# Kernel optimization log

Measured on AMD Instinct MI355X. Metric: run time of the kernel, lower is better.

Reference implementation:

```python
import jax, jax.numpy as jnp
import numpy as np

EPS = 1e-5  # BatchNorm1d default eps
N1, N2 = 4096, 4096


def _encoder(x, W1, b1, W2, b2, W3, b3, gamma, beta):
    # fc1: Linear(node_num,256)+ReLU; fc2: Linear(256,128)+ReLU; fc3: Linear(128,64)+BN(train-mode)+ReLU
    h = jax.nn.relu(x @ W1.T + b1)
    h = jax.nn.relu(h @ W2.T + b2)
    h = h @ W3.T + b3
    m = h.mean(axis=0)
    v = ((h - m) ** 2).mean(axis=0)  # biased variance, as BN training mode
    return jax.nn.relu((h - m) / jnp.sqrt(v + EPS) * gamma + beta)


def _self_attention(x, adj, alpha):
    # vectorized form of the per-node double loop:
    # tmp_i = (sum_{j: adj[i,j]==1} alpha[i,j] * x[j]) / degree_i + x[i]  if degree_i != 0 else 0
    mask = (adj == 1.0).astype(x.dtype)           # [N,N]
    deg = adj.sum(axis=1, keepdims=True)          # [N,1]
    agg = (mask * alpha) @ x                      # [N,64] masked SpMM
    return jnp.where(deg != 0, agg / deg + x, jnp.zeros((), x.dtype))


def setup_inputs() -> dict:
    key = jax.random.key(0)
    ks = jax.random.split(key, 20)
    d = {}
    d["x1"] = jax.random.normal(ks[0], (N1, N1), jnp.float32)
    d["x2"] = jax.random.normal(ks[1], (N2, N2), jnp.float32)
    d["adj1"] = jax.random.bernoulli(ks[2], 0.01, (N1, N1)).astype(jnp.float32)
    d["adj2"] = jax.random.bernoulli(ks[3], 0.01, (N2, N2)).astype(jnp.float32)
    def lin(k, fan_out, fan_in):
        bound = 1.0 / np.sqrt(fan_in)
        k1, k2 = jax.random.split(k)
        return (jax.random.uniform(k1, (fan_out, fan_in), jnp.float32, -bound, bound),
                jax.random.uniform(k2, (fan_out,), jnp.float32, -bound, bound))
    d["e1_W1"], d["e1_b1"] = lin(ks[4], 256, N1)
    d["e1_W2"], d["e1_b2"] = lin(ks[5], 128, 256)
    d["e1_W3"], d["e1_b3"] = lin(ks[6], 64, 128)
    d["e1_gamma"] = jnp.ones((64,), jnp.float32)
    d["e1_beta"] = jnp.zeros((64,), jnp.float32)
    d["e2_W1"], d["e2_b1"] = lin(ks[7], 256, N2)
    d["e2_W2"], d["e2_b2"] = lin(ks[8], 128, 256)
    d["e2_W3"], d["e2_b3"] = lin(ks[9], 64, 128)
    d["e2_gamma"] = jnp.ones((64,), jnp.float32)
    d["e2_beta"] = jnp.zeros((64,), jnp.float32)
    d["alpha1"] = jax.random.uniform(ks[10], (N1, N1), jnp.float32)
    d["alpha2"] = jax.random.uniform(ks[11], (N2, N2), jnp.float32)
    d["Wc"], d["bc"] = lin(ks[12], 2, (N1 + N2) * 64)
    return d


def reference(x1, x2, adj1, adj2,
              e1_W1, e1_b1, e1_W2, e1_b2, e1_W3, e1_b3, e1_gamma, e1_beta,
              e2_W1, e2_b1, e2_W2, e2_b2, e2_W3, e2_b3, e2_gamma, e2_beta,
              alpha1, alpha2, Wc, bc):
    h1 = _encoder(x1, e1_W1, e1_b1, e1_W2, e1_b2, e1_W3, e1_b3, e1_gamma, e1_beta)
    h2 = _encoder(x2, e2_W1, e2_b1, e2_W2, e2_b2, e2_W3, e2_b3, e2_gamma, e2_beta)
    h1 = _self_attention(h1, adj1, alpha1)
    h2 = _self_attention(h2, adj2, alpha2)
    feat = jnp.concatenate([h1, h2], axis=0).reshape(1, -1)  # [1,(N1+N2)*64]
    return feat @ Wc.T + bc  # [1,2] logits (softmax is defined but unused in forward)
```

## Files before the change

### kernel.cpp

```cpp
#include <hip/hip_runtime.h>
#include <cstddef>
#include <cstdint>


#define NN 4096
#define HDIM 64
#define ENC_OUT (NN * HDIM)

typedef _Float16 half8 __attribute__((ext_vector_type(8)));
typedef _Float16 half4 __attribute__((ext_vector_type(4)));
typedef float v4f __attribute__((ext_vector_type(4)));

__device__ __forceinline__ void gld_lds16(const void* g, void* l) {
    __builtin_amdgcn_global_load_lds(
        (const __attribute__((address_space(1))) void*)g,
        (__attribute__((address_space(3))) void*)l, 16, 0, 0);
}

struct GemmP {
    const void*     A[2];
    const _Float16* B[2];
    const float*    bias[2];
    void*           C[2];
};

__global__ __launch_bounds__(1024) void fc1_kernel(GemmP p)
{
    __shared__ char Bs[64 * 1024];

    const int tid = threadIdx.x;
    const int wave = tid >> 6, lane = tid & 63;
    const int l16 = lane & 15, quad = lane >> 4;
    const int kg = wave >> 2, ng = wave & 3;
    const int enc = blockIdx.y;
    const int m0 = blockIdx.x * 32;
    const int kOff = kg * 1024;
    constexpr int nsteps = 1024 / 32;

    const float* __restrict__ A = (const float*)p.A[enc];
    const _Float16* __restrict__ Bb =
        p.B[enc] + (size_t)(ng * 64 + l16) * NN + kOff + quad * 8;

    const size_t aoff0 = (size_t)(m0 + l16) * NN + kOff + quad * 8;
    const size_t aoff1 = aoff0 + (size_t)16 * NN;

    float4 nf0lo, nf0hi, nf1lo, nf1hi;
    auto loadA = [&](int s) {
        nf0lo = *(const float4*)(A + aoff0 + s * 32);
        nf0hi = *(const float4*)(A + aoff0 + s * 32 + 4);
        nf1lo = *(const float4*)(A + aoff1 + s * 32);
        nf1hi = *(const float4*)(A + aoff1 + s * 32 + 4);
    };

    v4f acc[2][4];
#pragma unroll
    for (int mi = 0; mi < 2; mi++)
#pragma unroll
        for (int ni = 0; ni < 4; ni++) acc[mi][ni] = (v4f){0.f, 0.f, 0.f, 0.f};

    loadA(0);

    for (int s = 0; s < nsteps; ++s) {
#pragma unroll
        for (int ni = 0; ni < 4; ni++)
            gld_lds16(Bb + (size_t)ni * 16 * NN + s * 32, &Bs[(wave * 4 + ni) * 1024]);
        __builtin_amdgcn_sched_barrier(0);

        half8 ca0, ca1;
        ca0[0] = (_Float16)nf0lo.x; ca0[1] = (_Float16)nf0lo.y;
        ca0[2] = (_Float16)nf0lo.z; ca0[3] = (_Float16)nf0lo.w;
        ca0[4] = (_Float16)nf0hi.x; ca0[5] = (_Float16)nf0hi.y;
        ca0[6] = (_Float16)nf0hi.z; ca0[7] = (_Float16)nf0hi.w;
        ca1[0] = (_Float16)nf1lo.x; ca1[1] = (_Float16)nf1lo.y;
        ca1[2] = (_Float16)nf1lo.z; ca1[3] = (_Float16)nf1lo.w;
        ca1[4] = (_Float16)nf1hi.x; ca1[5] = (_Float16)nf1hi.y;
        ca1[6] = (_Float16)nf1hi.z; ca1[7] = (_Float16)nf1hi.w;

        if (s + 1 < nsteps) {
            loadA(s + 1);
            __builtin_amdgcn_sched_barrier(0);
            __builtin_amdgcn_s_waitcnt(0x0F74);
        } else {
            __builtin_amdgcn_sched_barrier(0);
            __builtin_amdgcn_s_waitcnt(0x0F70);
        }
        __builtin_amdgcn_sched_barrier(0);

#pragma unroll
        for (int ni = 0; ni < 4; ni++) {
            half8 bf = *(const half8*)&Bs[(wave * 4 + ni) * 1024 + lane * 16];
            acc[0][ni] = __builtin_amdgcn_mfma_f32_16x16x32_f16(ca0, bf, acc[0][ni], 0, 0, 0);
            acc[1][ni] = __builtin_amdgcn_mfma_f32_16x16x32_f16(ca1, bf, acc[1][ni], 0, 0, 0);
        }
    }

    __syncthreads();

    if (kg >= 2) {
        const int sidx = (kg - 2) * 4 + ng;
#pragma unroll
        for (int mi = 0; mi < 2; mi++)
#pragma unroll
            for (int ni = 0; ni < 4; ni++)
                *(v4f*)&Bs[sidx * 8192 + (mi * 4 + ni) * 1024 + lane * 16] = acc[mi][ni];
    }
    __syncthreads();
    if (kg < 2) {
        const int sidx = kg * 4 + ng;
#pragma unroll
        for (int mi = 0; mi < 2; mi++)
#pragma unroll
            for (int ni = 0; ni < 4; ni++)
                acc[mi][ni] += *(const v4f*)&Bs[sidx * 8192 + (mi * 4 + ni) * 1024 + lane * 16];
    }
    __syncthreads();

    if (kg == 1) {
#pragma unroll
        for (int mi = 0; mi < 2; mi++)
#pragma unroll
            for (int ni = 0; ni < 4; ni++)
                *(v4f*)&Bs[ng * 8192 + (mi * 4 + ni) * 1024 + lane * 16] = acc[mi][ni];
    }
    __syncthreads();

    if (kg == 0) {
        _Float16* __restrict__ h1 = (_Float16*)p.C[enc];
        const float* __restrict__ bs = p.bias[enc];
#pragma unroll
        for (int mi = 0; mi < 2; mi++)
#pragma unroll
            for (int ni = 0; ni < 4; ni++) {
                v4f v = acc[mi][ni] + *(const v4f*)&Bs[ng * 8192 + (mi * 4 + ni) * 1024 + lane * 16];
                const int col = ng * 64 + ni * 16 + l16;
                const float b = bs[col];
#pragma unroll
                for (int i = 0; i < 4; i++) {
                    const int row = m0 + mi * 16 + quad * 4 + i;
                    h1[(size_t)row * 256 + col] = (_Float16)fmaxf(v[i] + b, 0.f);
                }
            }
    }
}

template<int NI, bool A16, int OUT, bool RELU>
__global__ __launch_bounds__(256) void gemm_kernel(GemmP p, int M, int lda, int Ksub)
{
    constexpr int N = NI * 64;
    __shared__ char Bs[NI * 4 * 1024];

    const int tid = threadIdx.x;
    const int wave = tid >> 6, lane = tid & 63;
    const int l16 = lane & 15, quad = lane >> 4;
    const int enc = blockIdx.z, split = blockIdx.x;
    const int m0 = blockIdx.y * 32;
    const int kOff = split * Ksub;
    const int nsteps = Ksub >> 5;

    const _Float16* __restrict__ Bp = p.B[enc];
    const char* Abase = (const char*)p.A[enc];

    const size_t aoff0 = (size_t)(m0 + l16) * lda + kOff + quad * 8;
    const size_t aoff1 = aoff0 + (size_t)16 * lda;

    half8 na0, na1;
    float4 nf0lo, nf0hi, nf1lo, nf1hi;
    auto loadA = [&](int s) {
        if constexpr (A16) {
            const _Float16* A = (const _Float16*)Abase;
            na0 = *(const half8*)(A + aoff0 + s * 32);
            na1 = *(const half8*)(A + aoff1 + s * 32);
        } else {
            const float* A = (const float*)Abase;
            nf0lo = *(const float4*)(A + aoff0 + s * 32);
            nf0hi = *(const float4*)(A + aoff0 + s * 32 + 4);
            nf1lo = *(const float4*)(A + aoff1 + s * 32);
            nf1hi = *(const float4*)(A + aoff1 + s * 32 + 4);
        }
    };

    v4f acc[2][NI];
#pragma unroll
    for (int mi = 0; mi < 2; mi++)
#pragma unroll
        for (int ni = 0; ni < NI; ni++) acc[mi][ni] = (v4f){0.f, 0.f, 0.f, 0.f};

    loadA(0);

    for (int s = 0; s < nsteps; ++s) {
#pragma unroll
        for (int ni = 0; ni < NI; ni++) {
            const int T = wave * NI + ni;
            const _Float16* g = Bp + (size_t)(T * 16 + l16) * lda + kOff + s * 32 + quad * 8;
            gld_lds16(g, &Bs[T * 1024]);
        }
        half8 ca0, ca1;
        if constexpr (A16) {
            ca0 = na0; ca1 = na1;
        } else {
            ca0[0] = (_Float16)nf0lo.x; ca0[1] = (_Float16)nf0lo.y;
            ca0[2] = (_Float16)nf0lo.z; ca0[3] = (_Float16)nf0lo.w;
            ca0[4] = (_Float16)nf0hi.x; ca0[5] = (_Float16)nf0hi.y;
            ca0[6] = (_Float16)nf0hi.z; ca0[7] = (_Float16)nf0hi.w;
            ca1[0] = (_Float16)nf1lo.x; ca1[1] = (_Float16)nf1lo.y;
            ca1[2] = (_Float16)nf1lo.z; ca1[3] = (_Float16)nf1lo.w;
            ca1[4] = (_Float16)nf1hi.x; ca1[5] = (_Float16)nf1hi.y;
            ca1[6] = (_Float16)nf1hi.z; ca1[7] = (_Float16)nf1hi.w;
        }
        if (s + 1 < nsteps) loadA(s + 1);

        __builtin_amdgcn_s_waitcnt(0x0F70);

#pragma unroll
        for (int ni = 0; ni < NI; ni++) {
            half8 bf = *(const half8*)&Bs[(wave * NI + ni) * 1024 + lane * 16];
            acc[0][ni] = __builtin_amdgcn_mfma_f32_16x16x32_f16(ca0, bf, acc[0][ni], 0, 0, 0);
            acc[1][ni] = __builtin_amdgcn_mfma_f32_16x16x32_f16(ca1, bf, acc[1][ni], 0, 0, 0);
        }
    }

#pragma unroll
    for (int mi = 0; mi < 2; mi++)
#pragma unroll
        for (int ni = 0; ni < NI; ni++) {
            const int col = wave * NI * 16 + ni * 16 + l16;
#pragma unroll
            for (int i = 0; i < 4; i++) {
                const int row = m0 + mi * 16 + quad * 4 + i;
                float v = acc[mi][ni][i];
                v += p.bias[enc][col];
                if (RELU) v = fmaxf(v, 0.f);
                if constexpr (OUT == 0)
                    ((_Float16*)p.C[enc])[(size_t)row * N + col] = (_Float16)v;
                else
                    ((float*)p.C[enc])[(size_t)row * N + col] = v;
            }
        }
}

struct CvtJob { const float* s; _Float16* d; int n4; };
struct CvtP { CvtJob j[6]; };

__global__ __launch_bounds__(256) void cvt_all_kernel(CvtP p)
{
    int i = blockIdx.x * 256 + threadIdx.x;
#pragma unroll
    for (int k = 0; k < 6; k++) {
        if (i < p.j[k].n4) {
            float4 v = ((const float4*)p.j[k].s)[i];
            half4 h;
            h[0] = (_Float16)v.x; h[1] = (_Float16)v.y;
            h[2] = (_Float16)v.z; h[3] = (_Float16)v.w;
            ((half4*)p.j[k].d)[i] = h;
            return;
        }
        i -= p.j[k].n4;
    }
}

__global__ __launch_bounds__(256) void bn_stat1_kernel(const float* __restrict__ h3,
                                                       float* __restrict__ bnp)
{
    const int enc = blockIdx.y, b = blockIdx.x;
    const int c = threadIdx.x & 63, rg = threadIdx.x >> 6;
    const float* h = h3 + (size_t)enc * ENC_OUT + (size_t)b * 128 * HDIM;
    float s = 0.f, q = 0.f;
    for (int r = rg; r < 128; r += 4) {
        float v = h[(size_t)r * HDIM + c];
        s += v; q += v * v;
    }
    __shared__ float ss[4][64], sq[4][64];
    ss[rg][c] = s; sq[rg][c] = q;
    __syncthreads();
    if (threadIdx.x < 64) {
        float S = ss[0][c] + ss[1][c] + ss[2][c] + ss[3][c];
        float Q = sq[0][c] + sq[1][c] + sq[2][c] + sq[3][c];
        bnp[(size_t)(enc * 32 + b) * 128 + c] = S;
        bnp[(size_t)(enc * 32 + b) * 128 + 64 + c] = Q;
    }
}

__global__ void bn_stat2_kernel(const float* __restrict__ bnp, float* __restrict__ stats)
{
    const int enc = blockIdx.x, c = threadIdx.x;
    float s = 0.f, q = 0.f;
    for (int b = 0; b < 32; b++) {
        s += bnp[(size_t)(enc * 32 + b) * 128 + c];
        q += bnp[(size_t)(enc * 32 + b) * 128 + 64 + c];
    }
    float mean = s * (1.f / NN);
    float var = q * (1.f / NN) - mean * mean;
    stats[enc * 128 + c] = mean;
    stats[enc * 128 + 64 + c] = rsqrtf(var + 1e-5f);
}

__global__ __launch_bounds__(256) void bn_apply_kernel(const float* __restrict__ h3,
                                                       const float* __restrict__ stats,
                                                       const float* __restrict__ g0,
                                                       const float* __restrict__ g1,
                                                       const float* __restrict__ be0,
                                                       const float* __restrict__ be1,
                                                       float* __restrict__ hn)
{
    const int idx = blockIdx.x * 256 + threadIdx.x;
    const int enc = idx >> 18;
    const int c = idx & 63;
    const float* g = enc ? g1 : g0;
    const float* be = enc ? be1 : be0;
    const float m = stats[enc * 128 + c];
    const float rs = stats[enc * 128 + 64 + c];
    float v = (h3[idx] - m) * rs * g[c] + be[c];
    hn[idx] = fmaxf(v, 0.f);
}

__global__ __launch_bounds__(256) void att_kernel(const float* __restrict__ adj1,
                                                  const float* __restrict__ adj2,
                                                  const float* __restrict__ al1,
                                                  const float* __restrict__ al2,
                                                  const float* __restrict__ hn,
                                                  float* __restrict__ out)
{
    const int enc = blockIdx.y;
    const float* adj = enc ? adj2 : adj1;
    const float* al = enc ? al2 : al1;
    const float* h = hn + (size_t)enc * ENC_OUT;
    float* o = out + (size_t)enc * ENC_OUT;
    const int i = blockIdx.x;
    const int tid = threadIdx.x;

    __shared__ int s_cnt;
    __shared__ int s_j[128];
    __shared__ float s_w[128];
    __shared__ float s_acc[4][64];

    if (tid == 0) s_cnt = 0;
    __syncthreads();

    const float* arow = adj + (size_t)i * NN;
    const int jb = tid * 16;
#pragma unroll
    for (int q = 0; q < 4; q++) {
        float4 a = *(const float4*)&arow[jb + q * 4];
        if (a.x == 1.f) { int p = atomicAdd(&s_cnt, 1); if (p < 128) s_j[p] = jb + q * 4 + 0; }
        if (a.y == 1.f) { int p = atomicAdd(&s_cnt, 1); if (p < 128) s_j[p] = jb + q * 4 + 1; }
        if (a.z == 1.f) { int p = atomicAdd(&s_cnt, 1); if (p < 128) s_j[p] = jb + q * 4 + 2; }
        if (a.w == 1.f) { int p = atomicAdd(&s_cnt, 1); if (p < 128) s_j[p] = jb + q * 4 + 3; }
    }
    __syncthreads();
    const int cnt = min(s_cnt, 128);

    const float* alrow = al + (size_t)i * NN;
    for (int t = tid; t < cnt; t += 256) s_w[t] = alrow[s_j[t]];
    __syncthreads();

    const int c = tid & 63;
    const int g = tid >> 6;
    float acc = 0.f;
    for (int t = g; t < cnt; t += 4) acc += s_w[t] * h[(size_t)s_j[t] * HDIM + c];
    s_acc[g][c] = acc;
    __syncthreads();

    if (tid < 64) {
        float r;
        if (cnt != 0) {
            r = (s_acc[0][c] + s_acc[1][c] + s_acc[2][c] + s_acc[3][c]) / (float)cnt
                + h[(size_t)i * HDIM + c];
        } else {
            r = 0.f;
        }
        o[(size_t)i * HDIM + c] = r;
    }
}

#define FDIM (2 * ENC_OUT)

__global__ __launch_bounds__(256) void final_partial_kernel(const float* __restrict__ feat,
                                                            const float* __restrict__ Wc,
                                                            float* __restrict__ partial)
{
    const int gt = blockIdx.x * 256 + threadIdx.x;
    float p0 = 0.f, p1 = 0.f;
    for (int f = gt; f < FDIM; f += 131072) {
        float x = feat[f];
        p0 += x * Wc[f];
        p1 += x * Wc[FDIM + f];
    }
    __shared__ float r0[256], r1[256];
    r0[threadIdx.x] = p0;
    r1[threadIdx.x] = p1;
    __syncthreads();
    for (int off = 128; off > 0; off >>= 1) {
        if (threadIdx.x < off) {
            r0[threadIdx.x] += r0[threadIdx.x + off];
            r1[threadIdx.x] += r1[threadIdx.x + off];
        }
        __syncthreads();
    }
    if (threadIdx.x == 0) {
        partial[blockIdx.x * 2 + 0] = r0[0];
        partial[blockIdx.x * 2 + 1] = r1[0];
    }
}

__global__ void final_reduce_kernel(const float* __restrict__ partial,
                                    const float* __restrict__ bc,
                                    float* __restrict__ out)
{
    const int t = threadIdx.x;
    if (t < 2) {
        float s = bc[t];
        for (int b = 0; b < 512; b++) s += partial[b * 2 + t];
        out[t] = s;
    }
}


extern "C" void kernel_launch(void* const* d_in, const int* in_sizes, int n_in,
                              void* d_out, int out_size, void* d_ws, size_t ws_size,
                              hipStream_t stream)
{
    const float* x1    = (const float*)d_in[0];
    const float* x2    = (const float*)d_in[1];
    const float* adj1  = (const float*)d_in[2];
    const float* adj2  = (const float*)d_in[3];
    const float* e1_W1 = (const float*)d_in[4];
    const float* e1_b1 = (const float*)d_in[5];
    const float* e1_W2 = (const float*)d_in[6];
    const float* e1_b2 = (const float*)d_in[7];
    const float* e1_W3 = (const float*)d_in[8];
    const float* e1_b3 = (const float*)d_in[9];
    const float* e1_g  = (const float*)d_in[10];
    const float* e1_be = (const float*)d_in[11];
    const float* e2_W1 = (const float*)d_in[12];
    const float* e2_b1 = (const float*)d_in[13];
    const float* e2_W2 = (const float*)d_in[14];
    const float* e2_b2 = (const float*)d_in[15];
    const float* e2_W3 = (const float*)d_in[16];
    const float* e2_b3 = (const float*)d_in[17];
    const float* e2_g  = (const float*)d_in[18];
    const float* e2_be = (const float*)d_in[19];
    const float* alpha1 = (const float*)d_in[20];
    const float* alpha2 = (const float*)d_in[21];
    const float* Wc    = (const float*)d_in[22];
    const float* bc    = (const float*)d_in[23];
    (void)in_sizes; (void)n_in; (void)out_size; (void)ws_size;

    char* w = (char*)d_ws;
    _Float16* W1h = (_Float16*)w;  w += (size_t)2 * 256 * NN * 2;
    _Float16* W2h = (_Float16*)w;  w += (size_t)2 * 128 * 256 * 2;
    _Float16* W3h = (_Float16*)w;  w += (size_t)2 * 64 * 128 * 2;
    _Float16* h1h = (_Float16*)w;  w += (size_t)2 * NN * 256 * 2;
    char* shared8 = w;             w += (size_t)8 * 1024 * 1024;
    float* bnp = (float*)w;        w += (size_t)2 * 32 * 128 * 4;
    float* stats = (float*)w;      w += 256 * 4;
    float* hpart = (float*)w;      w += 1024 * 4;

    _Float16* h2h  = (_Float16*)shared8;
    float* h3  = (float*)(shared8 + 2 * 1024 * 1024);
    float* hn  = (float*)(shared8 + 4 * 1024 * 1024);
    float* att = (float*)(shared8 + 6 * 1024 * 1024);

    const dim3 blk(256);

    CvtP cp;
    cp.j[0] = { e1_W1, W1h,             262144 };
    cp.j[1] = { e2_W1, W1h + 256 * NN,  262144 };
    cp.j[2] = { e1_W2, W2h,             8192 };
    cp.j[3] = { e2_W2, W2h + 128 * 256, 8192 };
    cp.j[4] = { e1_W3, W3h,             2048 };
    cp.j[5] = { e2_W3, W3h + 64 * 128,  2048 };
    cvt_all_kernel<<<dim3(2128), blk, 0, stream>>>(cp);

    GemmP p1 = { {x1, x2}, {W1h, W1h + 256 * NN}, {e1_b1, e2_b1},
                 {h1h, h1h + (size_t)NN * 256} };
    fc1_kernel<<<dim3(NN / 32, 2), dim3(1024), 0, stream>>>(p1);

    GemmP p2 = { {h1h, h1h + (size_t)NN * 256}, {W2h, W2h + 128 * 256}, {e1_b2, e2_b2},
                 {h2h, h2h + (size_t)NN * 128} };
    gemm_kernel<2, true, 0, true><<<dim3(1, NN / 32, 2), blk, 0, stream>>>(p2, NN, 256, 256);

    GemmP p3 = { {h2h, h2h + (size_t)NN * 128}, {W3h, W3h + 64 * 128}, {e1_b3, e2_b3},
                 {h3, h3 + ENC_OUT} };
    gemm_kernel<1, true, 1, false><<<dim3(1, NN / 32, 2), blk, 0, stream>>>(p3, NN, 128, 128);

    bn_stat1_kernel<<<dim3(32, 2), blk, 0, stream>>>(h3, bnp);
    bn_stat2_kernel<<<dim3(2), dim3(64), 0, stream>>>(bnp, stats);
    bn_apply_kernel<<<dim3(2 * ENC_OUT / 256), blk, 0, stream>>>(h3, stats, e1_g, e2_g,
                                                                 e1_be, e2_be, hn);

    att_kernel<<<dim3(NN, 2), blk, 0, stream>>>(adj1, adj2, alpha1, alpha2, hn, att);

    final_partial_kernel<<<dim3(512), blk, 0, stream>>>(att, Wc, hpart);
    final_reduce_kernel<<<dim3(1), dim3(64), 0, stream>>>(hpart, bc, (float*)d_out);
}
```

Baseline: 506.5 us.

## Stage fp32 A tiles through LDS with double-buffered fp16 conversion in fc1

fc1 now loads the fp32 A tile directly into LDS with global_load_lds, using a swizzled chunk order. Each wave converts its part to fp16 once into a shared double-buffered fp16 tile that all N-groups read, instead of every wave loading and converting its own A fragments. B fragments now go into registers with one-step-ahead prefetch, and A is prefetched two steps ahead. This cuts redundant global A loads and conversions, but adds a block-wide barrier on every k-step. Separately, the final 512-partial reduction is parallelised across 256 threads with a tree reduction in shared memory, replacing a two-thread serial loop.

```diff
diff --git a/kernel.cpp b/kernel.cpp
--- a/kernel.cpp
+++ b/kernel.cpp
@@ -24,9 +24,9 @@
     void*           C[2];
 };
 
-__global__ __launch_bounds__(1024) void fc1_kernel(GemmP p)
-{
-    __shared__ char Bs[64 * 1024];
+__global__ __launch_bounds__(1024, 4) void fc1_kernel(GemmP p)
+{
+    __shared__ char lds[64 * 1024];
 
     const int tid = threadIdx.x;
     const int wave = tid >> 6, lane = tid & 63;
@@ -35,63 +35,89 @@
     const int enc = blockIdx.y;
     const int m0 = blockIdx.x * 32;
     const int kOff = kg * 1024;
-    constexpr int nsteps = 1024 / 32;
+    constexpr int NS = 32;
 
     const float* __restrict__ A = (const float*)p.A[enc];
-    const _Float16* __restrict__ Bb =
-        p.B[enc] + (size_t)(ng * 64 + l16) * NN + kOff + quad * 8;
-
-    const size_t aoff0 = (size_t)(m0 + l16) * NN + kOff + quad * 8;
-    const size_t aoff1 = aoff0 + (size_t)16 * NN;
-
-    float4 nf0lo, nf0hi, nf1lo, nf1hi;
-    auto loadA = [&](int s) {
-        nf0lo = *(const float4*)(A + aoff0 + s * 32);
-        nf0hi = *(const float4*)(A + aoff0 + s * 32 + 4);
-        nf1lo = *(const float4*)(A + aoff1 + s * 32);
-        nf1hi = *(const float4*)(A + aoff1 + s * 32 + 4);
+    const _Float16* __restrict__ Bp = p.B[enc];
+
+    const int srow = ng * 8 + (lane >> 3);
+    const int schunk = (lane & 7) ^ ((lane >> 3) & 7);
+    const float* asrc0 = A + (size_t)(m0 + srow) * NN + kOff + schunk * 4;
+    char* f32base = &lds[kg * 8192 + ng * 1024];
+    char* f16kg   = &lds[32768 + kg * 4096];
+
+    const int f16woff = (schunk >> 1) * 512 + srow * 16 + (schunk & 1) * 8;
+
+    const int frag0 = quad * 512 + l16 * 16;
+    const int frag1 = quad * 512 + (16 + l16) * 16;
+
+    const _Float16* bsrc = Bp + (size_t)(ng * 64 + l16) * NN + kOff + quad * 8;
+
+    v4f acc[2][4];
+#pragma unroll
+    for (int mi = 0; mi < 2; mi++)
+#pragma unroll
+        for (int ni = 0; ni < 4; ni++) acc[mi][ni] = (v4f){0.f, 0.f, 0.f, 0.f};
+
+    half8 b0[4], b1[4];
+
+    gld_lds16(asrc0, f32base);
+#pragma unroll
+    for (int ni = 0; ni < 4; ni++)
+        b0[ni] = *(const half8*)(bsrc + (size_t)ni * 16 * NN);
+    gld_lds16(asrc0 + 32, f32base + 4096);
+    __builtin_amdgcn_sched_barrier(0);
+    __builtin_amdgcn_s_waitcnt(0x0F75);
+    __builtin_amdgcn_sched_barrier(0);
+    {
+        float4 f = *(const float4*)(f32base + lane * 16);
+        half4 h;
+        h[0] = (_Float16)f.x; h[1] = (_Float16)f.y;
+        h[2] = (_Float16)f.z; h[3] = (_Float16)f.w;
+        *(half4*)(f16kg + f16woff) = h;
+    }
+    __builtin_amdgcn_sched_barrier(0);
+    __builtin_amdgcn_s_waitcnt(0x3F7F & 0xC07F);
+    __builtin_amdgcn_sched_barrier(0);
+    __builtin_amdgcn_s_barrier();
+
+    auto body = [&](int s, half8* bcur, half8* bnxt) {
+        if (s + 1 < NS) {
+#pragma unroll
+            for (int ni = 0; ni < 4; ni++)
+                bnxt[ni] = *(const half8*)(bsrc + (size_t)ni * 16 * NN + (s + 1) * 32);
+        }
+        if (s + 2 < NS)
+            gld_lds16(asrc0 + (s + 2) * 32, f32base + ((s + 2) & 1) * 4096);
+        __builtin_amdgcn_sched_barrier(0);
+        if (s + 2 < NS)      __builtin_amdgcn_s_waitcnt(0x0F75);
+        else if (s + 1 < NS) __builtin_amdgcn_s_waitcnt(0x0F74);
+        else                 __builtin_amdgcn_s_waitcnt(0x0F70);
+        __builtin_amdgcn_sched_barrier(0);
+        if (s + 1 < NS) {
+            float4 f = *(const float4*)(f32base + ((s + 1) & 1) * 4096 + lane * 16);
+            half4 h;
+            h[0] = (_Float16)f.x; h[1] = (_Float16)f.y;
+            h[2] = (_Float16)f.z; h[3] = (_Float16)f.w;
+            *(half4*)(f16kg + ((s + 1) & 1) * 2048 + f16woff) = h;
+        }
+        const char* fb = f16kg + (s & 1) * 2048;
+        half8 ca0 = *(const half8*)(fb + frag0);
+        half8 ca1 = *(const half8*)(fb + frag1);
+#pragma unroll
+        for (int ni = 0; ni < 4; ni++) {
+            acc[0][ni] = __builtin_amdgcn_mfma_f32_16x16x32_f16(ca0, bcur[ni], acc[0][ni], 0, 0, 0);
+            acc[1][ni] = __builtin_amdgcn_mfma_f32_16x16x32_f16(ca1, bcur[ni], acc[1][ni], 0, 0, 0);
+        }
+        __builtin_amdgcn_sched_barrier(0);
+        __builtin_amdgcn_s_waitcnt(0xC07F);
+        __builtin_amdgcn_sched_barrier(0);
+        __builtin_amdgcn_s_barrier();
     };
 
-    v4f acc[2][4];
-#pragma unroll
-    for (int mi = 0; mi < 2; mi++)
-#pragma unroll
-        for (int ni = 0; ni < 4; ni++) acc[mi][ni] = (v4f){0.f, 0.f, 0.f, 0.f};
-
-    loadA(0);
-
-    for (int s = 0; s < nsteps; ++s) {
-#pragma unroll
-        for (int ni = 0; ni < 4; ni++)
-            gld_lds16(Bb + (size_t)ni * 16 * NN + s * 32, &Bs[(wave * 4 + ni) * 1024]);
-        __builtin_amdgcn_sched_barrier(0);
-
-        half8 ca0, ca1;
-        ca0[0] = (_Float16)nf0lo.x; ca0[1] = (_Float16)nf0lo.y;
-        ca0[2] = (_Float16)nf0lo.z; ca0[3] = (_Float16)nf0lo.w;
-        ca0[4] = (_Float16)nf0hi.x; ca0[5] = (_Float16)nf0hi.y;
-        ca0[6] = (_Float16)nf0hi.z; ca0[7] = (_Float16)nf0hi.w;
-        ca1[0] = (_Float16)nf1lo.x; ca1[1] = (_Float16)nf1lo.y;
-        ca1[2] = (_Float16)nf1lo.z; ca1[3] = (_Float16)nf1lo.w;
-        ca1[4] = (_Float16)nf1hi.x; ca1[5] = (_Float16)nf1hi.y;
-        ca1[6] = (_Float16)nf1hi.z; ca1[7] = (_Float16)nf1hi.w;
-
-        if (s + 1 < nsteps) {
-            loadA(s + 1);
-            __builtin_amdgcn_sched_barrier(0);
-            __builtin_amdgcn_s_waitcnt(0x0F74);
-        } else {
-            __builtin_amdgcn_sched_barrier(0);
-            __builtin_amdgcn_s_waitcnt(0x0F70);
-        }
-        __builtin_amdgcn_sched_barrier(0);
-
-#pragma unroll
-        for (int ni = 0; ni < 4; ni++) {
-            half8 bf = *(const half8*)&Bs[(wave * 4 + ni) * 1024 + lane * 16];
-            acc[0][ni] = __builtin_amdgcn_mfma_f32_16x16x32_f16(ca0, bf, acc[0][ni], 0, 0, 0);
-            acc[1][ni] = __builtin_amdgcn_mfma_f32_16x16x32_f16(ca1, bf, acc[1][ni], 0, 0, 0);
-        }
+    for (int s = 0; s < NS; s += 2) {
+        body(s, b0, b1);
+        body(s + 1, b1, b0);
     }
 
     __syncthreads();
@@ -102,7 +128,7 @@
         for (int mi = 0; mi < 2; mi++)
 #pragma unroll
             for (int ni = 0; ni < 4; ni++)
-                *(v4f*)&Bs[sidx * 8192 + (mi * 4 + ni) * 1024 + lane * 16] = acc[mi][ni];
+                *(v4f*)&lds[sidx * 8192 + (mi * 4 + ni) * 1024 + lane * 16] = acc[mi][ni];
     }
     __syncthreads();
     if (kg < 2) {
@@ -111,7 +137,7 @@
         for (int mi = 0; mi < 2; mi++)
 #pragma unroll
             for (int ni = 0; ni < 4; ni++)
-                acc[mi][ni] += *(const v4f*)&Bs[sidx * 8192 + (mi * 4 + ni) * 1024 + lane * 16];
+                acc[mi][ni] += *(const v4f*)&lds[sidx * 8192 + (mi * 4 + ni) * 1024 + lane * 16];
     }
     __syncthreads();
 
@@ -120,7 +146,7 @@
         for (int mi = 0; mi < 2; mi++)
 #pragma unroll
             for (int ni = 0; ni < 4; ni++)
-                *(v4f*)&Bs[ng * 8192 + (mi * 4 + ni) * 1024 + lane * 16] = acc[mi][ni];
+                *(v4f*)&lds[ng * 8192 + (mi * 4 + ni) * 1024 + lane * 16] = acc[mi][ni];
     }
     __syncthreads();
 
@@ -131,7 +157,7 @@
         for (int mi = 0; mi < 2; mi++)
 #pragma unroll
             for (int ni = 0; ni < 4; ni++) {
-                v4f v = acc[mi][ni] + *(const v4f*)&Bs[ng * 8192 + (mi * 4 + ni) * 1024 + lane * 16];
+                v4f v = acc[mi][ni] + *(const v4f*)&lds[ng * 8192 + (mi * 4 + ni) * 1024 + lane * 16];
                 const int col = ng * 64 + ni * 16 + l16;
                 const float b = bs[col];
 #pragma unroll
@@ -402,15 +428,27 @@
     }
 }
 
-__global__ void final_reduce_kernel(const float* __restrict__ partial,
-                                    const float* __restrict__ bc,
-                                    float* __restrict__ out)
+__global__ __launch_bounds__(256) void final_reduce_kernel(const float* __restrict__ partial,
+                                                           const float* __restrict__ bc,
+                                                           float* __restrict__ out)
 {
     const int t = threadIdx.x;
-    if (t < 2) {
-        float s = bc[t];
-        for (int b = 0; b < 512; b++) s += partial[b * 2 + t];
-        out[t] = s;
+    float2 v = ((const float2*)partial)[t];
+    float2 w = ((const float2*)partial)[t + 256];
+    __shared__ float r0[256], r1[256];
+    r0[t] = v.x + w.x;
+    r1[t] = v.y + w.y;
+    __syncthreads();
+    for (int off = 128; off > 0; off >>= 1) {
+        if (t < off) {
+            r0[t] += r0[t + off];
+            r1[t] += r1[t + off];
+        }
+        __syncthreads();
+    }
+    if (t == 0) {
+        out[0] = bc[0] + r0[0];
+        out[1] = bc[1] + r1[0];
     }
 }
 
@@ -491,5 +529,5 @@
     att_kernel<<<dim3(NN, 2), blk, 0, stream>>>(adj1, adj2, alpha1, alpha2, hn, att);
 
     final_partial_kernel<<<dim3(512), blk, 0, stream>>>(att, Wc, hpart);
-    final_reduce_kernel<<<dim3(1), dim3(64), 0, stream>>>(hpart, bc, (float*)d_out);
-}
+    final_reduce_kernel<<<dim3(1), blk, 0, stream>>>(hpart, bc, (float*)d_out);
+}
```

After: 469.8 us. -7.2%, faster.
